# Performance work log

Hardware: AMD Instinct MI355X
Metric: run time of the kernel (lower is better)

Reference implementation:

```python
import jax, jax.numpy as jnp
import numpy as np

B, N, DIM, HEAD = 32, 1024, 512, 8
W_SP = 32  # sqrt(N), query spatial side
SCALE = DIM ** (-0.5)  # original uses full dim, not head_dim
EPS = 1e-5


def setup_inputs() -> dict:
    key = jax.random.key(0)
    ks = jax.random.split(key, 7)
    feats = jax.random.normal(ks[0], (B, N, DIM), dtype=jnp.float32)
    W_q = jax.random.normal(ks[1], (DIM, DIM), dtype=jnp.float32) * (DIM ** -0.5)
    conv_w = jax.random.normal(ks[2], (2 * DIM, DIM, 3, 3), dtype=jnp.float32) * ((DIM * 9) ** -0.5)
    conv_b = jnp.zeros((2 * DIM,), dtype=jnp.float32)
    ln_gamma = jnp.ones((2 * DIM,), dtype=jnp.float32)
    ln_beta = jnp.zeros((2 * DIM,), dtype=jnp.float32)
    W_out = jax.random.normal(ks[3], (DIM, DIM), dtype=jnp.float32) * (DIM ** -0.5)
    return {"feats": feats, "W_q": W_q, "conv_w": conv_w, "conv_b": conv_b,
            "ln_gamma": ln_gamma, "ln_beta": ln_beta, "W_out": W_out}


def reference(feats, W_q, conv_w, conv_b, ln_gamma, ln_beta, W_out):
    b, n, dim = feats.shape
    h = HEAD
    d = dim // h
    # trans_kv: 'b (w h) c -> b c w h' -> conv2d(dim->2dim, k3 s2 p1) -> 'b c w h -> b (w h) c' -> LN
    x = feats.reshape(b, W_SP, W_SP, dim).transpose(0, 3, 1, 2)  # NCHW
    kv = jax.lax.conv_general_dilated(
        x, conv_w, window_strides=(2, 2), padding=((1, 1), (1, 1)),
        dimension_numbers=("NCHW", "OIHW", "NCHW"))
    kv = kv + conv_b[None, :, None, None]          # [b, 2dim, w2, w2]
    m = kv.shape[2] * kv.shape[3]
    kv = kv.reshape(b, 2 * dim, m).transpose(0, 2, 1)  # [b, m, 2dim]
    mu = jnp.mean(kv, axis=-1, keepdims=True)
    var = jnp.var(kv, axis=-1, keepdims=True)
    kv = (kv - mu) * jax.lax.rsqrt(var + EPS) * ln_gamma + ln_beta
    k, v = jnp.split(kv, 2, axis=-1)               # each [b, m, dim]
    q = feats @ W_q.T                               # [b, n, dim]
    q = q.reshape(b, n, h, d)
    k = k.reshape(b, m, h, d)
    v = v.reshape(b, m, h, d)
    alpha = jnp.einsum("bihd,bjhd->bhij", q, k) * SCALE  # [b, h, n, m]
    # NOTE: original computes Conv(alpha) into att, then overwrites with softmax(alpha);
    # the Conv block is dead code w.r.t. the output.
    att = jax.nn.softmax(alpha, axis=-1)
    out = jnp.einsum("bhij,bjhd->bhid", att, v)    # [b, h, n, d]
    out = out.transpose(0, 2, 1, 3).reshape(b, n, dim)
    out = out @ W_out.T                             # fc_out linear (dropout=identity in eval)
    return out
```

## Files before the change

### kernel.cpp

```cpp
#include <hip/hip_runtime.h>
#include <hip/hip_bf16.h>
#include <math.h>

#define B_    32
#define N_    1024
#define DIM_  512
#define HEAD_ 8
#define HD_   64
#define WSP   32
#define M2    256
#define CDIM  1024
#define KCONV 4608
#define EPS_  1e-5f
#define SCALE_ 0.044194173824159216f
#define PW    34

typedef __attribute__((ext_vector_type(8))) short bf16x8;
typedef __attribute__((ext_vector_type(4))) float f32x4_t;
typedef const __attribute__((address_space(1))) void gas_t;
typedef __attribute__((address_space(3))) void las_t;

__device__ __forceinline__ ushort f2b(float x) {
  __hip_bfloat16 h = __float2bfloat16(x);
  return *reinterpret_cast<const ushort*>(&h);
}

__global__ __launch_bounds__(256) void misc_prep_kernel(
    ushort* __restrict__ featsp, const float* __restrict__ W_q,
    ushort* __restrict__ wqb, const float* __restrict__ W_out,
    ushort* __restrict__ woutb) {
  int blk = blockIdx.x;
  if (blk < 1056) {
    int t = blk * 256 + threadIdx.x;
    int b = t / 8448, r = t - b * 8448;
    int cell = r >> 6, ic8 = (r & 63) * 8;
    int iw, ih;
    if (cell < 34)      { iw = 0;  ih = cell; }
    else if (cell < 68) { iw = 33; ih = cell - 34; }
    else { int e = cell - 68; iw = 1 + (e >> 1); ih = (e & 1) * 33; }
    bf16x8 z = {};
    *reinterpret_cast<bf16x8*>(&featsp[(((size_t)b * PW + iw) * PW + ih) * 512 + ic8]) = z;
  } else if (blk < 1312) {
    int i = (blk - 1056) * 256 + threadIdx.x;
    float4 v = reinterpret_cast<const float4*>(W_q)[i];
    ushort4 o;
    o.x = f2b(v.x); o.y = f2b(v.y); o.z = f2b(v.z); o.w = f2b(v.w);
    reinterpret_cast<ushort4*>(wqb)[i] = o;
  } else {
    int i = (blk - 1312) * 256 + threadIdx.x;
    float4 v = reinterpret_cast<const float4*>(W_out)[i];
    ushort4 o;
    o.x = f2b(v.x); o.y = f2b(v.y); o.z = f2b(v.z); o.w = f2b(v.w);
    reinterpret_cast<ushort4*>(woutb)[i] = o;
  }
}

__global__ __launch_bounds__(256) void cast_featsp_kernel(
    const float* __restrict__ feats, ushort* __restrict__ featsp) {
  int i = blockIdx.x * 256 + threadIdx.x;
  int e = i * 4;
  int b = e >> 19, r = e & 524287;
  int n = r >> 9, ic = r & 511;
  int iw = n >> 5, ih = n & 31;
  float4 v = reinterpret_cast<const float4*>(feats)[i];
  ushort4 o;
  o.x = f2b(v.x); o.y = f2b(v.y); o.z = f2b(v.z); o.w = f2b(v.w);
  size_t dst = (((size_t)b * PW + iw + 1) * PW + ih + 1) * 512 + ic;
  *reinterpret_cast<ushort4*>(&featsp[dst]) = o;
}

__global__ __launch_bounds__(256) void permute_convw_kernel(
    const float* __restrict__ in, ushort* __restrict__ out) {
  int oc = blockIdx.y;
  int idx = blockIdx.x * 256 + threadIdx.x;
  int tap = idx >> 9, ic = idx & 511;
  out[(size_t)oc * KCONV + idx] = f2b(in[(size_t)oc * KCONV + ic * 9 + tap]);
}

template<int MODE>
__device__ __forceinline__ void gemm_body(
    ushort (*As)[128][32], ushort (*Bs)[128][32],
    int l, int nbn, int nwg,
    const ushort* __restrict__ A, const ushort* __restrict__ featsp,
    const ushort* __restrict__ Bw, float* __restrict__ Cf,
    ushort* __restrict__ Cb, const float* __restrict__ bias,
    int M, int N, int K) {
  const int tid = threadIdx.x;
  const int lane = tid & 63, wid = tid >> 6;
  const int wr = wid >> 1, wc = wid & 1;
  const int v = (l & 7) * (nwg >> 3) + (l >> 3);
  const int bm = (v / nbn) * 128, bn = (v % nbn) * 128;
  const int lrow = lane & 15, lk = lane >> 4;
  const int swz = (lrow >> 1) & 3;

  f32x4_t acc[4][4] = {};

  auto stage = [&](int buf, int kt) {
    int k0 = kt << 5;
#pragma unroll
    for (int it = 0; it < 2; ++it) {
      int idx = it * 256 + tid;
      int row = idx >> 2;
      int c = (((idx & 3) ^ ((idx >> 3) & 3))) * 8;
      const ushort* ga;
      if (MODE == 0) {
        ga = &A[(size_t)(bm + row) * K + k0 + c];
      } else if (MODE == 1) {
        int p = bm + row;
        int b = p >> 10, n = p & 1023;
        int iw = n >> 5, ih = n & 31;
        ga = &featsp[(((size_t)b * PW + iw + 1) * PW + ih + 1) * 512 + k0 + c];
      } else {
        int p = bm + row;
        int b = p >> 8, sp = p & 255;
        int w2 = sp >> 4, h2 = sp & 15;
        int kk = k0 + c;
        int tap = kk >> 9, ic = kk & 511;
        int kh = tap / 3, kw = tap - 3 * kh;
        ga = &featsp[(((size_t)b * PW + 2 * w2 + kh) * PW + 2 * h2 + kw) * 512 + ic];
      }
      __builtin_amdgcn_global_load_lds((gas_t*)ga,
          (las_t*)(&As[buf][0][0] + (size_t)idx * 8), 16, 0, 0);
      const ushort* gb = &Bw[(size_t)(bn + row) * K + k0 + c];
      __builtin_amdgcn_global_load_lds((gas_t*)gb,
          (las_t*)(&Bs[buf][0][0] + (size_t)idx * 8), 16, 0, 0);
    }
  };

  stage(0, 0);
  const int NT = K >> 5;
  for (int kt = 0; kt < NT; ++kt) {
    int cur = kt & 1;
    if (kt + 1 < NT) {
      stage(cur ^ 1, kt + 1);
      asm volatile("s_waitcnt vmcnt(4)" ::: "memory");
    } else {
      asm volatile("s_waitcnt vmcnt(0)" ::: "memory");
    }
    __builtin_amdgcn_s_barrier();
    __builtin_amdgcn_sched_barrier(0);
    bf16x8 aF[4], bF[4];
#pragma unroll
    for (int m = 0; m < 4; ++m)
      aF[m] = *reinterpret_cast<const bf16x8*>(
          &As[cur][wr * 64 + m * 16 + lrow][(lk ^ swz) * 8]);
#pragma unroll
    for (int n = 0; n < 4; ++n)
      bF[n] = *reinterpret_cast<const bf16x8*>(
          &Bs[cur][wc * 64 + n * 16 + lrow][(lk ^ swz) * 8]);
#pragma unroll
    for (int m = 0; m < 4; ++m)
#pragma unroll
      for (int n = 0; n < 4; ++n)
        acc[m][n] = __builtin_amdgcn_mfma_f32_16x16x32_bf16(
            aF[m], bF[n], acc[m][n], 0, 0, 0);
    __builtin_amdgcn_sched_barrier(0);
    __builtin_amdgcn_s_barrier();
  }

#pragma unroll
  for (int m = 0; m < 4; ++m) {
#pragma unroll
    for (int n = 0; n < 4; ++n) {
      int col = bn + wc * 64 + n * 16 + lrow;
#pragma unroll
      for (int r = 0; r < 4; ++r) {
        int row = bm + wr * 64 + m * 16 + lk * 4 + r;
        float v2 = acc[m][n][r];
        if (MODE == 2) v2 += bias[col];
        if (MODE == 1) Cb[(size_t)row * N + col] = f2b(v2);
        else Cf[(size_t)row * N + col] = v2;
      }
    }
  }
}

__global__ __launch_bounds__(256) void conv_kernel(
    const ushort* __restrict__ featsp, const ushort* __restrict__ convwb,
    const float* __restrict__ conv_b, float* __restrict__ kvf) {
  __shared__ ushort As[2][128][32];
  __shared__ ushort Bs[2][128][32];
  int l = blockIdx.y * gridDim.x + blockIdx.x;
  gemm_body<2>(As, Bs, l, gridDim.x, gridDim.x * gridDim.y,
               nullptr, featsp, convwb, kvf, nullptr, conv_b,
               B_ * M2, CDIM, KCONV);
}

__global__ __launch_bounds__(256) void qproj_kernel(
    const ushort* __restrict__ featsp, const ushort* __restrict__ wqb,
    ushort* __restrict__ qb) {
  __shared__ ushort As[2][128][32];
  __shared__ ushort Bs[2][128][32];
  int l = blockIdx.y * gridDim.x + blockIdx.x;
  gemm_body<1>(As, Bs, l, gridDim.x, gridDim.x * gridDim.y,
               nullptr, featsp, wqb, nullptr, qb, nullptr,
               B_ * N_, DIM_, DIM_);
}

__global__ __launch_bounds__(256) void gemm0_kernel(
    const ushort* __restrict__ A, const ushort* __restrict__ Bw,
    float* __restrict__ Cf, int M, int N, int K) {
  __shared__ ushort As[2][128][32];
  __shared__ ushort Bs[2][128][32];
  int l = blockIdx.y * gridDim.x + blockIdx.x;
  gemm_body<0>(As, Bs, l, gridDim.x, gridDim.x * gridDim.y,
               A, nullptr, Bw, Cf, nullptr, nullptr, M, N, K);
}

__global__ __launch_bounds__(256) void ln_kernel(
    const float* __restrict__ kvin, const float* __restrict__ gamma,
    const float* __restrict__ beta, ushort* __restrict__ Kb,
    ushort* __restrict__ Vt) {
  const int p = blockIdx.x, tid = threadIdx.x;
  float4 x = reinterpret_cast<const float4*>(kvin + (size_t)p * CDIM)[tid];
  float s = x.x + x.y + x.z + x.w;
  float ss = x.x * x.x + x.y * x.y + x.z * x.z + x.w * x.w;
#pragma unroll
  for (int off = 32; off > 0; off >>= 1) {
    s += __shfl_down(s, off);
    ss += __shfl_down(ss, off);
  }
  __shared__ float sb[4], ssb[4];
  if ((tid & 63) == 0) { sb[tid >> 6] = s; ssb[tid >> 6] = ss; }
  __syncthreads();
  float tot = sb[0] + sb[1] + sb[2] + sb[3];
  float tot2 = ssb[0] + ssb[1] + ssb[2] + ssb[3];
  float mu = tot * (1.f / CDIM);
  float var = tot2 * (1.f / CDIM) - mu * mu;
  float rstd = rsqrtf(var + EPS_);
  float4 g = reinterpret_cast<const float4*>(gamma)[tid];
  float4 bb = reinterpret_cast<const float4*>(beta)[tid];
  ushort o0 = f2b((x.x - mu) * rstd * g.x + bb.x);
  ushort o1 = f2b((x.y - mu) * rstd * g.y + bb.y);
  ushort o2 = f2b((x.z - mu) * rstd * g.z + bb.z);
  ushort o3 = f2b((x.w - mu) * rstd * g.w + bb.w);
  int b = p >> 8, j = p & 255;
  int c = tid * 4;
  if (c < DIM_) {
    int h = c >> 6, d = c & 63;
    ushort4 o = make_ushort4(o0, o1, o2, o3);
    *reinterpret_cast<ushort4*>(&Kb[(((size_t)(b * 8 + h)) * M2 + j) * HD_ + d]) = o;
  } else {
    int c2 = c - DIM_;
    int h = c2 >> 6, d = c2 & 63;
    size_t base = ((size_t)(b * 8 + h) * HD_ + d) * M2 + j;
    Vt[base]           = o0;
    Vt[base + M2]      = o1;
    Vt[base + 2 * M2]  = o2;
    Vt[base + 3 * M2]  = o3;
  }
}

__global__ __launch_bounds__(512, 2) void attn_mfma_kernel(
    const ushort* __restrict__ qb, const ushort* __restrict__ Kb,
    const ushort* __restrict__ Vt, ushort* __restrict__ attob) {
  __shared__ __align__(16) char lds[131072];
  char* lp = lds;
  const int tid = threadIdx.x;
  const int lane = tid & 63, wid = tid >> 6;
  const int lr = lane & 15, lk = lane >> 4;
  const int bh = blockIdx.x;
  const int b = bh >> 3, h = bh & 7;

  auto ks_byte = [](int j, int d) -> int {
    return (j << 7) + (((d << 1)) ^ ((j & 7) << 4));
  };
  auto vt_byte = [](int d, int j) -> int {
    return 32768 + (d << 9) + (((j << 1)) ^ ((d & 7) << 4));
  };
  auto p_byte = [](int w, int q4, int kv) -> int {
    return 65536 + (w << 13) + (q4 << 9) + (((kv << 1)) ^ ((q4 & 7) << 4));
  };

  const ushort* Khead  = Kb + (size_t)bh * M2 * HD_;
  const ushort* Vthead = Vt + (size_t)bh * HD_ * M2;

#pragma unroll
  for (int it = 0; it < 4; ++it) {
    int o = (it * 512 + tid) * 16;
    int j = o >> 7, c = (o >> 4) & 7;
    int cl = c ^ (j & 7);
    __builtin_amdgcn_global_load_lds((gas_t*)(Khead + j * HD_ + cl * 8),
        (las_t*)(lp + o), 16, 0, 0);
  }
#pragma unroll
  for (int it = 0; it < 4; ++it) {
    int o = (it * 512 + tid) * 16;
    int d = o >> 9, c = (o >> 4) & 31;
    int cl = c ^ (d & 7);
    __builtin_amdgcn_global_load_lds((gas_t*)(Vthead + d * M2 + cl * 8),
        (las_t*)(lp + 32768 + o), 16, 0, 0);
  }

  __syncthreads();

  for (int qp = 0; qp < 4; ++qp) {
    const int qbase = qp * 256 + wid * 32;
    bf16x8 qf[2][2];
#pragma unroll
    for (int mf = 0; mf < 2; ++mf)
#pragma unroll
      for (int ks = 0; ks < 2; ++ks)
        qf[mf][ks] = *reinterpret_cast<const bf16x8*>(
            qb + ((size_t)(b * N_ + qbase + mf * 16 + lr)) * DIM_ + h * HD_ + ks * 32 + lk * 8);

    f32x4_t sacc[2][16] = {};
    __builtin_amdgcn_s_setprio(1);
#pragma unroll
    for (int ks = 0; ks < 2; ++ks) {
#pragma unroll
      for (int nj = 0; nj < 16; ++nj) {
        bf16x8 kf = *reinterpret_cast<const bf16x8*>(
            lp + ks_byte(nj * 16 + lr, ks * 32 + lk * 8));
        sacc[0][nj] = __builtin_amdgcn_mfma_f32_16x16x32_bf16(qf[0][ks], kf, sacc[0][nj], 0, 0, 0);
        sacc[1][nj] = __builtin_amdgcn_mfma_f32_16x16x32_bf16(qf[1][ks], kf, sacc[1][nj], 0, 0, 0);
      }
    }
    __builtin_amdgcn_s_setprio(0);

    float linv[2][4];
    f32x4_t oacc[2][4] = {};
#pragma unroll
    for (int mf = 0; mf < 2; ++mf) {
#pragma unroll
      for (int r = 0; r < 4; ++r) {
        float pv[16];
        float sum = 0.f;
#pragma unroll
        for (int nj = 0; nj < 16; ++nj) {
          pv[nj] = __expf(sacc[mf][nj][r] * SCALE_);
          sum += pv[nj];
        }
        sum += __shfl_xor(sum, 1);
        sum += __shfl_xor(sum, 2);
        sum += __shfl_xor(sum, 4);
        sum += __shfl_xor(sum, 8);
        linv[mf][r] = 1.f / sum;
        int q4 = lk * 4 + r;
#pragma unroll
        for (int nj = 0; nj < 16; ++nj)
          *reinterpret_cast<ushort*>(lp + p_byte(wid, q4, nj * 16 + lr)) = f2b(pv[nj]);
      }
      __builtin_amdgcn_s_setprio(1);
#pragma unroll
      for (int ks2 = 0; ks2 < 8; ++ks2) {
        bf16x8 pf = *reinterpret_cast<const bf16x8*>(
            lp + p_byte(wid, lr, ks2 * 32 + lk * 8));
#pragma unroll
        for (int df = 0; df < 4; ++df) {
          bf16x8 vf = *reinterpret_cast<const bf16x8*>(
              lp + vt_byte(df * 16 + lr, ks2 * 32 + lk * 8));
          oacc[mf][df] = __builtin_amdgcn_mfma_f32_16x16x32_bf16(pf, vf, oacc[mf][df], 0, 0, 0);
        }
      }
      __builtin_amdgcn_s_setprio(0);
    }

#pragma unroll
    for (int mf = 0; mf < 2; ++mf)
#pragma unroll
      for (int df = 0; df < 4; ++df)
#pragma unroll
        for (int r = 0; r < 4; ++r) {
          int qrow = qbase + mf * 16 + lk * 4 + r;
          int dcol = df * 16 + lr;
          float val = oacc[mf][df][r] * linv[mf][r];
          attob[((size_t)(b * N_ + qrow)) * DIM_ + h * HD_ + dcol] = f2b(val);
        }
  }
}

extern "C" void kernel_launch(void* const* d_in, const int* in_sizes, int n_in,
                              void* d_out, int out_size, void* d_ws, size_t ws_size,
                              hipStream_t stream) {
  const float* feats  = (const float*)d_in[0];
  const float* W_q    = (const float*)d_in[1];
  const float* conv_w = (const float*)d_in[2];
  const float* conv_b = (const float*)d_in[3];
  const float* ln_g   = (const float*)d_in[4];
  const float* ln_b   = (const float*)d_in[5];
  const float* W_out  = (const float*)d_in[6];
  float* out = (float*)d_out;

  const size_t FP_ELEMS = (size_t)B_ * PW * PW * DIM_;
  char* ws = (char*)d_ws;
  ushort* featsp = (ushort*)ws;  ws += FP_ELEMS * 2;
  ushort* qb     = (ushort*)ws;  ws += (size_t)B_ * N_ * DIM_ * 2;
  ushort* attob  = (ushort*)ws;  ws += (size_t)B_ * N_ * DIM_ * 2;
  float*  kvf    = (float*)ws;   ws += (size_t)B_ * M2 * CDIM * 4;
  ushort* convwb = (ushort*)ws;  ws += (size_t)CDIM * KCONV * 2;
  ushort* wqb    = (ushort*)ws;  ws += (size_t)DIM_ * DIM_ * 2;
  ushort* woutb  = (ushort*)ws;  ws += (size_t)DIM_ * DIM_ * 2;
  ushort* Kb     = (ushort*)ws;  ws += (size_t)B_ * HEAD_ * M2 * HD_ * 2;
  ushort* Vt     = (ushort*)ws;  ws += (size_t)B_ * HEAD_ * M2 * HD_ * 2;

  misc_prep_kernel<<<1568, 256, 0, stream>>>(featsp, W_q, wqb, W_out, woutb);
  cast_featsp_kernel<<<16384, 256, 0, stream>>>(feats, featsp);
  permute_convw_kernel<<<dim3(18, CDIM), 256, 0, stream>>>(conv_w, convwb);

  qproj_kernel<<<dim3(DIM_ / 128, (B_ * N_) / 128), 256, 0, stream>>>(
      featsp, wqb, qb);

  conv_kernel<<<dim3(CDIM / 128, (B_ * M2) / 128), 256, 0, stream>>>(
      featsp, convwb, conv_b, kvf);

  ln_kernel<<<B_ * M2, 256, 0, stream>>>(kvf, ln_g, ln_b, Kb, Vt);

  attn_mfma_kernel<<<B_ * HEAD_, 512, 0, stream>>>(qb, Kb, Vt, attob);

  gemm0_kernel<<<dim3(DIM_ / 128, (B_ * N_) / 128), 256, 0, stream>>>(
      attob, woutb, out, B_ * N_, DIM_, DIM_);
}
```

Measured before the change: 270.5 us.

## Replace conv GEMM with 256x256-tile split-K kernel and sum partials in LayerNorm

The implicit-GEMM conv moves from 128x128 tiles with 256 threads to 256x256 tiles with 512 threads and a K-step of 64, using an XOR-swizzled LDS layout. K is split in two across blockIdx.z, giving 256 workgroups. The second partial is written into the attention-output buffer, which is free at that point, and the LayerNorm kernel adds the two partials while loading. The goal is more data reuse per tile and better CU fill. The cost is larger LDS and register use per block and an extra fp32 partial buffer that must be written and read.

```diff
diff --git a/kernel.cpp b/kernel.cpp
--- a/kernel.cpp
+++ b/kernel.cpp
@@ -11,6 +11,7 @@
 #define M2    256
 #define CDIM  1024
 #define KCONV 4608
+#define KHALF 2304
 #define EPS_  1e-5f
 #define SCALE_ 0.044194173824159216f
 #define PW    34
@@ -77,14 +78,114 @@
   out[(size_t)oc * KCONV + idx] = f2b(in[(size_t)oc * KCONV + ic * 9 + tap]);
 }
 
+__global__ __launch_bounds__(512, 2) void conv256_kernel(
+    const ushort* __restrict__ featsp, const ushort* __restrict__ convwb,
+    const float* __restrict__ conv_b, float* __restrict__ kvf,
+    float* __restrict__ kvp1) {
+  __shared__ __align__(16) ushort lds[2][32768];
+  const int tid = threadIdx.x;
+  const int lane = tid & 63, wid = tid >> 6;
+  const int wr = wid >> 2, wc = wid & 3;
+  const int lrow = lane & 15, lk = lane >> 4;
+  const int kz = blockIdx.z;
+  const int koff = kz * KHALF;
+
+  const int l = blockIdx.y * gridDim.x + blockIdx.x;
+  const int v = (l & 7) * 16 + (l >> 3);
+  const int bm = (v >> 2) * 256;
+  const int bn = (v & 3) * 256;
+  const int bimg = bm >> 8;
+
+  f32x4_t acc[8][4] = {};
+
+  auto stage = [&](int buf, int kt) {
+    int k0 = koff + (kt << 6);
+#pragma unroll
+    for (int i = 0; i < 4; ++i) {
+      int s = i * 512 + tid;
+      int row = s >> 3, ch = s & 7;
+      int cl = ch ^ (row & 7);
+      int kk = k0 + cl * 8;
+      int tap = kk >> 9, ic = kk & 511;
+      int kh = tap / 3, kw = tap - 3 * kh;
+      int w2 = row >> 4, h2 = row & 15;
+      const ushort* ga = &featsp[(((size_t)bimg * PW + 2 * w2 + kh) * PW + 2 * h2 + kw) * 512 + ic];
+      __builtin_amdgcn_global_load_lds((gas_t*)ga,
+          (las_t*)(&lds[buf][0] + (size_t)s * 8), 16, 0, 0);
+    }
+#pragma unroll
+    for (int i = 0; i < 4; ++i) {
+      int s = i * 512 + tid;
+      int row = s >> 3, ch = s & 7;
+      int cl = ch ^ (row & 7);
+      const ushort* gb = &convwb[(size_t)(bn + row) * KCONV + k0 + cl * 8];
+      __builtin_amdgcn_global_load_lds((gas_t*)gb,
+          (las_t*)(&lds[buf][16384] + (size_t)s * 8), 16, 0, 0);
+    }
+  };
+
+  const int NT = KHALF >> 6;
+  stage(0, 0);
+  for (int kt = 0; kt < NT; ++kt) {
+    int cur = kt & 1;
+    if (kt + 1 < NT) {
+      stage(cur ^ 1, kt + 1);
+      asm volatile("s_waitcnt vmcnt(8)" ::: "memory");
+    } else {
+      asm volatile("s_waitcnt vmcnt(0)" ::: "memory");
+    }
+    __builtin_amdgcn_s_barrier();
+    __builtin_amdgcn_sched_barrier(0);
+#pragma unroll
+    for (int kk = 0; kk < 2; ++kk) {
+      bf16x8 aF[8], bF[4];
+#pragma unroll
+      for (int m = 0; m < 8; ++m) {
+        int row = wr * 128 + m * 16 + lrow;
+        int ch = (kk * 4 + lk) ^ (row & 7);
+        aF[m] = *reinterpret_cast<const bf16x8*>(&lds[cur][row * 64 + ch * 8]);
+      }
+#pragma unroll
+      for (int n = 0; n < 4; ++n) {
+        int row = wc * 64 + n * 16 + lrow;
+        int ch = (kk * 4 + lk) ^ (row & 7);
+        bF[n] = *reinterpret_cast<const bf16x8*>(&lds[cur][16384 + row * 64 + ch * 8]);
+      }
+#pragma unroll
+      for (int m = 0; m < 8; ++m)
+#pragma unroll
+        for (int n = 0; n < 4; ++n)
+          acc[m][n] = __builtin_amdgcn_mfma_f32_16x16x32_bf16(
+              aF[m], bF[n], acc[m][n], 0, 0, 0);
+    }
+    __builtin_amdgcn_sched_barrier(0);
+    __builtin_amdgcn_s_barrier();
+  }
+
+  float* Co = kz ? kvp1 : kvf;
+#pragma unroll
+  for (int m = 0; m < 8; ++m) {
+#pragma unroll
+    for (int n = 0; n < 4; ++n) {
+      int col = bn + wc * 64 + n * 16 + lrow;
+#pragma unroll
+      for (int r = 0; r < 4; ++r) {
+        int row = bm + wr * 128 + m * 16 + lk * 4 + r;
+        float v2 = acc[m][n][r];
+        if (kz == 0) v2 += conv_b[col];
+        Co[(size_t)row * CDIM + col] = v2;
+      }
+    }
+  }
+}
+
 template<int MODE>
 __device__ __forceinline__ void gemm_body(
     ushort (*As)[128][32], ushort (*Bs)[128][32],
     int l, int nbn, int nwg,
     const ushort* __restrict__ A, const ushort* __restrict__ featsp,
     const ushort* __restrict__ Bw, float* __restrict__ Cf,
-    ushort* __restrict__ Cb, const float* __restrict__ bias,
-    int M, int N, int K) {
+    ushort* __restrict__ Cb, int M, int N, int K) {
   const int tid = threadIdx.x;
   const int lane = tid & 63, wid = tid >> 6;
   const int wr = wid >> 1, wc = wid & 1;
@@ -105,19 +206,11 @@
       const ushort* ga;
       if (MODE == 0) {
         ga = &A[(size_t)(bm + row) * K + k0 + c];
-      } else if (MODE == 1) {
+      } else {
         int p = bm + row;
         int b = p >> 10, n = p & 1023;
         int iw = n >> 5, ih = n & 31;
         ga = &featsp[(((size_t)b * PW + iw + 1) * PW + ih + 1) * 512 + k0 + c];
-      } else {
-        int p = bm + row;
-        int b = p >> 8, sp = p & 255;
-        int w2 = sp >> 4, h2 = sp & 15;
-        int kk = k0 + c;
-        int tap = kk >> 9, ic = kk & 511;
-        int kh = tap / 3, kw = tap - 3 * kh;
-        ga = &featsp[(((size_t)b * PW + 2 * w2 + kh) * PW + 2 * h2 + kw) * 512 + ic];
       }
       __builtin_amdgcn_global_load_lds((gas_t*)ga,
           (las_t*)(&As[buf][0][0] + (size_t)idx * 8), 16, 0, 0);
@@ -167,23 +260,11 @@
       for (int r = 0; r < 4; ++r) {
         int row = bm + wr * 64 + m * 16 + lk * 4 + r;
         float v2 = acc[m][n][r];
-        if (MODE == 2) v2 += bias[col];
         if (MODE == 1) Cb[(size_t)row * N + col] = f2b(v2);
         else Cf[(size_t)row * N + col] = v2;
       }
     }
   }
-}
-
-__global__ __launch_bounds__(256) void conv_kernel(
-    const ushort* __restrict__ featsp, const ushort* __restrict__ convwb,
-    const float* __restrict__ conv_b, float* __restrict__ kvf) {
-  __shared__ ushort As[2][128][32];
-  __shared__ ushort Bs[2][128][32];
-  int l = blockIdx.y * gridDim.x + blockIdx.x;
-  gemm_body<2>(As, Bs, l, gridDim.x, gridDim.x * gridDim.y,
-               nullptr, featsp, convwb, kvf, nullptr, conv_b,
-               B_ * M2, CDIM, KCONV);
 }
 
 __global__ __launch_bounds__(256) void qproj_kernel(
@@ -193,8 +274,7 @@
   __shared__ ushort Bs[2][128][32];
   int l = blockIdx.y * gridDim.x + blockIdx.x;
   gemm_body<1>(As, Bs, l, gridDim.x, gridDim.x * gridDim.y,
-               nullptr, featsp, wqb, nullptr, qb, nullptr,
-               B_ * N_, DIM_, DIM_);
+               nullptr, featsp, wqb, nullptr, qb, B_ * N_, DIM_, DIM_);
 }
 
 __global__ __launch_bounds__(256) void gemm0_kernel(
@@ -204,15 +284,17 @@
   __shared__ ushort Bs[2][128][32];
   int l = blockIdx.y * gridDim.x + blockIdx.x;
   gemm_body<0>(As, Bs, l, gridDim.x, gridDim.x * gridDim.y,
-               A, nullptr, Bw, Cf, nullptr, nullptr, M, N, K);
+               A, nullptr, Bw, Cf, nullptr, M, N, K);
 }
 
 __global__ __launch_bounds__(256) void ln_kernel(
-    const float* __restrict__ kvin, const float* __restrict__ gamma,
-    const float* __restrict__ beta, ushort* __restrict__ Kb,
-    ushort* __restrict__ Vt) {
+    const float* __restrict__ kvp0, const float* __restrict__ kvp1,
+    const float* __restrict__ gamma, const float* __restrict__ beta,
+    ushort* __restrict__ Kb, ushort* __restrict__ Vt) {
   const int p = blockIdx.x, tid = threadIdx.x;
-  float4 x = reinterpret_cast<const float4*>(kvin + (size_t)p * CDIM)[tid];
+  float4 a = reinterpret_cast<const float4*>(kvp0 + (size_t)p * CDIM)[tid];
+  float4 b4 = reinterpret_cast<const float4*>(kvp1 + (size_t)p * CDIM)[tid];
+  float4 x = make_float4(a.x + b4.x, a.y + b4.y, a.z + b4.z, a.w + b4.w);
   float s = x.x + x.y + x.z + x.w;
   float ss = x.x * x.x + x.y * x.y + x.z * x.z + x.w * x.w;
 #pragma unroll
@@ -393,6 +475,7 @@
   ushort* woutb  = (ushort*)ws;  ws += (size_t)DIM_ * DIM_ * 2;
   ushort* Kb     = (ushort*)ws;  ws += (size_t)B_ * HEAD_ * M2 * HD_ * 2;
   ushort* Vt     = (ushort*)ws;  ws += (size_t)B_ * HEAD_ * M2 * HD_ * 2;
+  float* kvp1 = (float*)attob;
 
   misc_prep_kernel<<<1568, 256, 0, stream>>>(featsp, W_q, wqb, W_out, woutb);
   cast_featsp_kernel<<<16384, 256, 0, stream>>>(feats, featsp);
@@ -401,10 +484,10 @@
   qproj_kernel<<<dim3(DIM_ / 128, (B_ * N_) / 128), 256, 0, stream>>>(
       featsp, wqb, qb);
 
-  conv_kernel<<<dim3(CDIM / 128, (B_ * M2) / 128), 256, 0, stream>>>(
-      featsp, convwb, conv_b, kvf);
-
-  ln_kernel<<<B_ * M2, 256, 0, stream>>>(kvf, ln_g, ln_b, Kb, Vt);
+  conv256_kernel<<<dim3(CDIM / 256, (B_ * M2) / 256, 2), 512, 0, stream>>>(
+      featsp, convwb, conv_b, kvf, kvp1);
+
+  ln_kernel<<<B_ * M2, 256, 0, stream>>>(kvf, kvp1, ln_g, ln_b, Kb, Vt);
 
   attn_mfma_kernel<<<B_ * HEAD_, 512, 0, stream>>>(qb, Kb, Vt, attob);
 
```

After: 259.9 us. 3.9% less time.
